# Kernel optimization log

Measured on AMD Instinct MI355X. Metric: run time of the kernel, lower is better.

The kernel has to match this reference:

```python
import jax, jax.numpy as jnp
import numpy as np

EPS = 1e-5

def _ln(x, g, b):
    m = jnp.mean(x, axis=-1, keepdims=True)
    v = jnp.var(x, axis=-1, keepdims=True)
    return (x - m) * jax.lax.rsqrt(v + EPS) * g + b

def _gelu(x):
    return jax.nn.gelu(x, approximate=False)  # torch nn.GELU default is exact erf

def setup_inputs() -> dict:
    key = jax.random.key(0)
    B, N, D, H = 4, 1024, 128, 12
    HID = H * D
    ks = jax.random.split(key, 16)
    s = lambda k, sh, fan: jax.random.normal(k, sh, jnp.float32) * (fan ** -0.5)
    return {
        "x": jax.random.normal(ks[0], (B, N, D), jnp.float32),
        # project: LN(D) -> Linear(D,HID) -> GELU -> Linear(HID,HID)
        "ln1_g": jnp.ones((D,), jnp.float32), "ln1_b": jnp.zeros((D,), jnp.float32),
        "W1": s(ks[1], (D, HID), D), "b1": jnp.zeros((HID,), jnp.float32),
        "W2": s(ks[2], (HID, HID), HID), "b2": jnp.zeros((HID,), jnp.float32),
        # shared Attention(inc=D, outc=D)
        "aln_g": jnp.ones((D,), jnp.float32), "aln_b": jnp.zeros((D,), jnp.float32),
        "Wqkv": s(ks[3], (D, 3 * D), D), "bqkv": jnp.zeros((3 * D,), jnp.float32),
        "Wl": s(ks[4], (D, D), D), "bl": jnp.zeros((D,), jnp.float32),
        # out_proj: LN(HID) -> Linear(HID, D) -> GELU
        "lno_g": jnp.ones((HID,), jnp.float32), "lno_b": jnp.zeros((HID,), jnp.float32),
        "Wo": s(ks[5], (HID, D), HID), "bo": jnp.zeros((D,), jnp.float32),
    }

def reference(x, ln1_g, ln1_b, W1, b1, W2, b2,
              aln_g, aln_b, Wqkv, bqkv, Wl, bl,
              lno_g, lno_b, Wo, bo):
    B, N, D = x.shape
    # project (dropout is identity in eval mode)
    h = _ln(x, ln1_g, ln1_b)
    h = _gelu(h @ W1 + b1)
    h = h @ W2 + b2                      # [B, N, H*D]
    H = h.shape[-1] // D
    # chunk along last dim into H features of width D; fold heads into batch
    f = h.reshape(B, N, H, D).transpose(0, 2, 1, 3).reshape(B * H, N, D)
    # shared Attention applied to each head-chunk
    a = _ln(f, aln_g, aln_b)
    qkv = a @ Wqkv + bqkv
    q, k, v = jnp.split(qkv, 3, axis=-1)
    scores = jax.nn.softmax(jnp.einsum('bnd,bmd->bnm', q, k) * (D ** -0.5), axis=-1)
    o = jnp.einsum('bnm,bmd->bnd', scores, v)
    o = o @ Wl + bl
    o = _gelu(o + f)                     # [B*H, N, D]
    # concat heads back along last dim
    feats = o.reshape(B, H, N, D).transpose(0, 2, 1, 3).reshape(B, N, H * D)
    out = _gelu(_ln(feats, lno_g, lno_b) @ Wo + bo)
    return out
```

## Files before the change

### kernel.cpp

```cpp
#include <hip/hip_runtime.h>
#include <stdint.h>

typedef unsigned short u16;
typedef __attribute__((ext_vector_type(8))) short short8;
typedef __attribute__((ext_vector_type(4))) float floatx4;

__device__ inline float b2f(u16 u) {
  union { uint32_t i; float f; } x; x.i = ((uint32_t)u) << 16; return x.f;
}
__device__ inline u16 f2b(float f) {
  union { float f; uint32_t i; } x; x.f = f;
  uint32_t r = (x.i + 0x7FFFu + ((x.i >> 16) & 1u)) >> 16;
  return (u16)r;
}
__device__ inline float gelu_f(float v) {
  return 0.5f * v * (1.0f + erff(v * 0.70710678118654752440f));
}

#define MFMA16(a, b, c) __builtin_amdgcn_mfma_f32_16x16x32_bf16((a), (b), (c), 0, 0, 0)

__device__ __forceinline__ void gl2lds16(const u16* g, u16* l) {
  __builtin_amdgcn_global_load_lds(
      (const __attribute__((address_space(1))) uint32_t*)(uintptr_t)g,
      (__attribute__((address_space(3))) uint32_t*)(uint32_t)(uintptr_t)l,
      16, 0, 0);
}

__global__ __launch_bounds__(256)
void tpose_all_kernel(const float* __restrict__ W1, const float* __restrict__ W2,
                      const float* __restrict__ Wqkv, const float* __restrict__ Wl,
                      const float* __restrict__ Wo,
                      u16* __restrict__ w1t, u16* __restrict__ w2t,
                      u16* __restrict__ wqkvt, u16* __restrict__ wlt,
                      u16* __restrict__ wot) {
  int id = blockIdx.x;
  const float* src; u16* dst; int R, C, bx, by;
  if (id < 2304)      { src = W2;   dst = w2t;   R = 1536; C = 1536; bx = (id % 48) * 32; by = (id / 48) * 32; }
  else if (id < 2496) { id -= 2304; src = W1;   dst = w1t;   R = 128;  C = 1536; bx = (id % 48) * 32; by = (id / 48) * 32; }
  else if (id < 2688) { id -= 2496; src = Wo;   dst = wot;   R = 1536; C = 128;  bx = (id % 4) * 32;  by = (id / 4) * 32; }
  else if (id < 2736) { id -= 2688; src = Wqkv; dst = wqkvt; R = 128;  C = 384;  bx = (id % 12) * 32; by = (id / 12) * 32; }
  else                { id -= 2736; src = Wl;   dst = wlt;   R = 128;  C = 128;  bx = (id % 4) * 32;  by = (id / 4) * 32; }
  __shared__ u16 t[32][33];
  int tx = threadIdx.x & 31, ty = threadIdx.x >> 5;
  for (int i = 0; i < 32; i += 8)
    t[ty + i][tx] = f2b(src[(size_t)(by + ty + i) * C + bx + tx]);
  __syncthreads();
  for (int i = 0; i < 32; i += 8)
    dst[(size_t)(bx + ty + i) * R + by + tx] = t[tx][ty + i];
}

__global__ __launch_bounds__(256)
void ln128_f32_kernel(const float* __restrict__ X, const float* __restrict__ g,
                      const float* __restrict__ bb, u16* __restrict__ Y) {
  int tid = threadIdx.x, w = tid >> 6, lane = tid & 63;
  int row = blockIdx.x * 4 + w;
  const float* xr = X + (size_t)row * 128;
  float2 xv = *(const float2*)(xr + lane * 2);
  float x0 = xv.x, x1 = xv.y;
  float s = x0 + x1, s2 = x0 * x0 + x1 * x1;
  for (int m = 1; m < 64; m <<= 1) { s += __shfl_xor(s, m, 64); s2 += __shfl_xor(s2, m, 64); }
  float mean = s * (1.0f / 128.0f);
  float var = s2 * (1.0f / 128.0f) - mean * mean;
  float rstd = 1.0f / sqrtf(var + 1e-5f);
  float2 gv = *(const float2*)(g + lane * 2);
  float2 bv = *(const float2*)(bb + lane * 2);
  float y0 = (x0 - mean) * rstd * gv.x + bv.x;
  float y1 = (x1 - mean) * rstd * gv.y + bv.y;
  *(uint32_t*)(Y + (size_t)row * 128 + lane * 2) =
      (uint32_t)f2b(y0) | ((uint32_t)f2b(y1) << 16);
}

__global__ __launch_bounds__(256)
void ln128_perm_kernel(const u16* __restrict__ X, const float* __restrict__ g,
                       const float* __restrict__ bb, u16* __restrict__ Y) {
  int tid = threadIdx.x, w = tid >> 6, lane = tid & 63;
  int rid = blockIdx.x * 4 + w;
  int bh = rid >> 10, n = rid & 1023;
  int b = bh / 12, h = bh % 12;
  const u16* xr = X + ((size_t)(b * 1024 + n)) * 1536 + h * 128;
  uint32_t u = *(const uint32_t*)(xr + lane * 2);
  float x0 = b2f(u & 0xffff), x1 = b2f(u >> 16);
  float s = x0 + x1, s2 = x0 * x0 + x1 * x1;
  for (int m = 1; m < 64; m <<= 1) { s += __shfl_xor(s, m, 64); s2 += __shfl_xor(s2, m, 64); }
  float mean = s * (1.0f / 128.0f);
  float var = s2 * (1.0f / 128.0f) - mean * mean;
  float rstd = 1.0f / sqrtf(var + 1e-5f);
  float2 gv = *(const float2*)(g + lane * 2);
  float2 bv = *(const float2*)(bb + lane * 2);
  float y0 = (x0 - mean) * rstd * gv.x + bv.x;
  float y1 = (x1 - mean) * rstd * gv.y + bv.y;
  *(uint32_t*)(Y + (size_t)rid * 128 + lane * 2) =
      (uint32_t)f2b(y0) | ((uint32_t)f2b(y1) << 16);
}

__global__ __launch_bounds__(256)
void ln1536_kernel(const u16* __restrict__ X, const float* __restrict__ g,
                   const float* __restrict__ bb, u16* __restrict__ Y) {
  int row = blockIdx.x, tid = threadIdx.x;
  const u16* xr = X + (size_t)row * 1536;
  uint32_t u0 = *(const uint32_t*)(xr + tid * 6);
  uint32_t u1 = *(const uint32_t*)(xr + tid * 6 + 2);
  uint32_t u2 = *(const uint32_t*)(xr + tid * 6 + 4);
  float v[6] = { b2f(u0 & 0xffff), b2f(u0 >> 16), b2f(u1 & 0xffff),
                 b2f(u1 >> 16),    b2f(u2 & 0xffff), b2f(u2 >> 16) };
  float s = 0.f, s2 = 0.f;
  for (int j = 0; j < 6; j++) { s += v[j]; s2 += v[j] * v[j]; }
  for (int m = 1; m < 64; m <<= 1) { s += __shfl_xor(s, m, 64); s2 += __shfl_xor(s2, m, 64); }
  __shared__ float red[8];
  int w = tid >> 6, lane = tid & 63;
  if (lane == 0) { red[w] = s; red[4 + w] = s2; }
  __syncthreads();
  s = red[0] + red[1] + red[2] + red[3];
  s2 = red[4] + red[5] + red[6] + red[7];
  float mean = s * (1.0f / 1536.0f);
  float var = s2 * (1.0f / 1536.0f) - mean * mean;
  float rstd = 1.0f / sqrtf(var + 1e-5f);
  uint32_t o[3];
  for (int p = 0; p < 3; p++) {
    int c = tid * 6 + p * 2;
    float y0 = (v[p * 2] - mean) * rstd * g[c] + bb[c];
    float y1 = (v[p * 2 + 1] - mean) * rstd * g[c + 1] + bb[c + 1];
    o[p] = (uint32_t)f2b(y0) | ((uint32_t)f2b(y1) << 16);
  }
  u16* yr = Y + (size_t)row * 1536 + tid * 6;
  *(uint32_t*)(yr) = o[0];
  *(uint32_t*)(yr + 2) = o[1];
  *(uint32_t*)(yr + 4) = o[2];
}

__global__ __launch_bounds__(256)
void qkv_kernel(const u16* __restrict__ A, const u16* __restrict__ BT,
                const float* __restrict__ bias, u16* __restrict__ qkv,
                u16* __restrict__ vT) {
  const int K = 128;
  __shared__ __align__(16) u16 abuf[128 * 32];
  __shared__ __align__(16) u16 bbuf[128 * 32];
  int tid = threadIdx.x;
  int w = tid >> 6, lane = tid & 63, ln = lane & 15, quad = lane >> 4;
  int bm = blockIdx.x * 128, bn = blockIdx.y * 128;
  int wr = w >> 1, wc = w & 1;
  floatx4 acc[4][4] = {};
  for (int k0 = 0; k0 < K; k0 += 32) {
    __syncthreads();
    for (int rd = 0; rd < 2; rd++) {
      int c = tid + rd * 256;
      int row = c >> 2, col = (c & 3) * 8;
      gl2lds16(A + (size_t)(bm + row) * K + k0 + col, abuf + c * 8);
      gl2lds16(BT + (size_t)(bn + row) * K + k0 + col, bbuf + c * 8);
    }
    __syncthreads();
    short8 af[4], bf[4];
    for (int i = 0; i < 4; i++)
      af[i] = *(const short8*)(abuf + (wr * 64 + i * 16 + ln) * 32 + quad * 8);
    for (int j = 0; j < 4; j++)
      bf[j] = *(const short8*)(bbuf + (wc * 64 + j * 16 + ln) * 32 + quad * 8);
    for (int i = 0; i < 4; i++)
      for (int j = 0; j < 4; j++)
        acc[i][j] = MFMA16(af[i], bf[j], acc[i][j]);
  }
  if (blockIdx.y < 2) {
    for (int i = 0; i < 4; i++) {
      int row0 = bm + wr * 64 + i * 16 + quad * 4;
      for (int j = 0; j < 4; j++) {
        int col = bn + wc * 64 + j * 16 + ln;
        float bv = bias[col];
        for (int r = 0; r < 4; r++)
          qkv[(size_t)(row0 + r) * 256 + col] = f2b(acc[i][j][r] + bv);
      }
    }
  } else {
    int bh = bm >> 10;
    int nb = bm & 1023;
    u16* vp = vT + (size_t)bh * 128 * 1024;
    for (int i = 0; i < 4; i++) {
      int n0 = nb + wr * 64 + i * 16 + quad * 4;
      for (int j = 0; j < 4; j++) {
        int d = wc * 64 + j * 16 + ln;
        float bv = bias[256 + d];
        u16 tmp[4];
        for (int r = 0; r < 4; r++) tmp[r] = f2b(acc[i][j][r] + bv);
        *(uint2*)(vp + (size_t)d * 1024 + n0) = *(const uint2*)tmp;
      }
    }
  }
}

template <int GELU, int RES, typename OUTT>
__global__ __launch_bounds__(256)
void gemm64_kernel(const u16* __restrict__ A, const u16* __restrict__ BT,
                   const float* __restrict__ bias, const u16* __restrict__ res,
                   OUTT* __restrict__ C, int M, int N, int K) {
  __shared__ __align__(16) u16 abuf[64 * 32];
  __shared__ __align__(16) u16 bbuf[128 * 32];
  int tid = threadIdx.x;
  int w = tid >> 6, lane = tid & 63, ln = lane & 15, quad = lane >> 4;
  int bm = blockIdx.x * 64, bn = blockIdx.y * 128;
  floatx4 acc[4][2] = {};
  for (int k0 = 0; k0 < K; k0 += 32) {
    __syncthreads();
    for (int rd = 0; rd < 2; rd++) {
      int c = tid + rd * 256;
      int row = c >> 2, col = (c & 3) * 8;
      gl2lds16(BT + (size_t)(bn + row) * K + k0 + col, bbuf + c * 8);
    }
    {
      int c = tid;
      int row = c >> 2, col = (c & 3) * 8;
      gl2lds16(A + (size_t)(bm + row) * K + k0 + col, abuf + c * 8);
    }
    __syncthreads();
    short8 af[4], bf[2];
    for (int i = 0; i < 4; i++)
      af[i] = *(const short8*)(abuf + (i * 16 + ln) * 32 + quad * 8);
    for (int j = 0; j < 2; j++)
      bf[j] = *(const short8*)(bbuf + (w * 32 + j * 16 + ln) * 32 + quad * 8);
    for (int i = 0; i < 4; i++)
      for (int j = 0; j < 2; j++)
        acc[i][j] = MFMA16(af[i], bf[j], acc[i][j]);
  }
  for (int i = 0; i < 4; i++) {
    int row0 = bm + i * 16 + quad * 4;
    for (int j = 0; j < 2; j++) {
      int col = bn + w * 32 + j * 16 + ln;
      float bv = bias[col];
      for (int r = 0; r < 4; r++) {
        float v = acc[i][j][r] + bv;
        if (RES) v += b2f(res[(size_t)(row0 + r) * N + col]);
        if (GELU) v = gelu_f(v);
        if constexpr (sizeof(OUTT) == 2)
          C[(size_t)(row0 + r) * N + col] = f2b(v);
        else
          C[(size_t)(row0 + r) * N + col] = v;
      }
    }
  }
}

template <int GELU, int RES, typename OUTT>
__global__ __launch_bounds__(256)
void gemm64b_kernel(const u16* __restrict__ A, const u16* __restrict__ BT,
                    const float* __restrict__ bias, const u16* __restrict__ res,
                    OUTT* __restrict__ C, int M, int N, int K) {
  __shared__ __align__(16) u16 abuf[2 * 64 * 32];
  __shared__ __align__(16) u16 bbuf[2 * 128 * 32];
  int tid = threadIdx.x;
  int w = tid >> 6, lane = tid & 63, ln = lane & 15, quad = lane >> 4;
  int bm = blockIdx.x * 64, bn = blockIdx.y * 128;
  floatx4 acc[4][2] = {};
  for (int k0 = 0; k0 < K; k0 += 64) {
    __syncthreads();
    for (int ks = 0; ks < 2; ks++) {
      {
        int c = tid;
        int row = c >> 2, cc = c & 3;
        gl2lds16(A + (size_t)(bm + row) * K + k0 + ks * 32 + cc * 8,
                 abuf + ks * 2048 + c * 8);
      }
      for (int rd = 0; rd < 2; rd++) {
        int c = tid + rd * 256;
        int row = c >> 2, cc = c & 3;
        gl2lds16(BT + (size_t)(bn + row) * K + k0 + ks * 32 + cc * 8,
                 bbuf + ks * 4096 + c * 8);
      }
    }
    __syncthreads();
    short8 af[2][4], bf[2][2];
    for (int ks = 0; ks < 2; ks++) {
      for (int i = 0; i < 4; i++)
        af[ks][i] = *(const short8*)(abuf + ks * 2048 + (i * 16 + ln) * 32 + quad * 8);
      for (int j = 0; j < 2; j++)
        bf[ks][j] = *(const short8*)(bbuf + ks * 4096 + (w * 32 + j * 16 + ln) * 32 + quad * 8);
    }
    for (int i = 0; i < 4; i++)
      for (int j = 0; j < 2; j++) {
        acc[i][j] = MFMA16(af[0][i], bf[0][j], acc[i][j]);
        acc[i][j] = MFMA16(af[1][i], bf[1][j], acc[i][j]);
      }
  }
  for (int i = 0; i < 4; i++) {
    int row0 = bm + i * 16 + quad * 4;
    for (int j = 0; j < 2; j++) {
      int col = bn + w * 32 + j * 16 + ln;
      float bv = bias[col];
      for (int r = 0; r < 4; r++) {
        float v = acc[i][j][r] + bv;
        if (RES) v += b2f(res[(size_t)(row0 + r) * N + col]);
        if (GELU) v = gelu_f(v);
        if constexpr (sizeof(OUTT) == 2)
          C[(size_t)(row0 + r) * N + col] = f2b(v);
        else
          C[(size_t)(row0 + r) * N + col] = v;
      }
    }
  }
}

__global__ __launch_bounds__(256)
void gemmwl_kernel(const u16* __restrict__ A, const u16* __restrict__ BT,
                   const float* __restrict__ bias, const u16* __restrict__ res,
                   u16* __restrict__ feats) {
  const int K = 128;
  __shared__ __align__(16) u16 abuf[64 * 32];
  __shared__ __align__(16) u16 bbuf[128 * 32];
  int tid = threadIdx.x;
  int w = tid >> 6, lane = tid & 63, ln = lane & 15, quad = lane >> 4;
  int bm = blockIdx.x * 64;
  floatx4 acc[4][2] = {};
  for (int k0 = 0; k0 < K; k0 += 32) {
    __syncthreads();
    for (int rd = 0; rd < 2; rd++) {
      int c = tid + rd * 256;
      int row = c >> 2, col = (c & 3) * 8;
      gl2lds16(BT + (size_t)row * K + k0 + col, bbuf + c * 8);
    }
    {
      int c = tid;
      int row = c >> 2, col = (c & 3) * 8;
      gl2lds16(A + (size_t)(bm + row) * K + k0 + col, abuf + c * 8);
    }
    __syncthreads();
    short8 af[4], bf[2];
    for (int i = 0; i < 4; i++)
      af[i] = *(const short8*)(abuf + (i * 16 + ln) * 32 + quad * 8);
    for (int j = 0; j < 2; j++)
      bf[j] = *(const short8*)(bbuf + (w * 32 + j * 16 + ln) * 32 + quad * 8);
    for (int i = 0; i < 4; i++)
      for (int j = 0; j < 2; j++)
        acc[i][j] = MFMA16(af[i], bf[j], acc[i][j]);
  }
  int bh = bm >> 10, nb = bm & 1023;
  int b = bh / 12, hh = bh % 12;
  size_t obase = ((size_t)b * 1024) * 1536 + hh * 128;
  for (int i = 0; i < 4; i++) {
    int n0 = nb + i * 16 + quad * 4;
    for (int j = 0; j < 2; j++) {
      int col = w * 32 + j * 16 + ln;
      float bv = bias[col];
      for (int r = 0; r < 4; r++) {
        size_t idx = obase + (size_t)(n0 + r) * 1536 + col;
        float v = acc[i][j][r] + bv + b2f(res[idx]);
        feats[idx] = f2b(gelu_f(v));
      }
    }
  }
}

__global__ __launch_bounds__(256)
void gemm64_part_kernel(const u16* __restrict__ A, const u16* __restrict__ BT,
                        float* __restrict__ pws, int Kfull, int kspan) {
  __shared__ __align__(16) u16 abuf[64 * 32];
  __shared__ __align__(16) u16 bbuf[128 * 32];
  int tid = threadIdx.x;
  int w = tid >> 6, lane = tid & 63, ln = lane & 15, quad = lane >> 4;
  int bm = blockIdx.x * 64;
  int kbeg = blockIdx.y * kspan, kend = kbeg + kspan;
  float* Cp = pws + (size_t)blockIdx.y * 4096 * 128;
  floatx4 acc[4][2] = {};
  for (int k0 = kbeg; k0 < kend; k0 += 32) {
    __syncthreads();
    for (int rd = 0; rd < 2; rd++) {
      int c = tid + rd * 256;
      int row = c >> 2, col = (c & 3) * 8;
      gl2lds16(BT + (size_t)row * Kfull + k0 + col, bbuf + c * 8);
    }
    {
      int c = tid;
      int row = c >> 2, col = (c & 3) * 8;
      gl2lds16(A + (size_t)(bm + row) * Kfull + k0 + col, abuf + c * 8);
    }
    __syncthreads();
    short8 af[4], bf[2];
    for (int i = 0; i < 4; i++)
      af[i] = *(const short8*)(abuf + (i * 16 + ln) * 32 + quad * 8);
    for (int j = 0; j < 2; j++)
      bf[j] = *(const short8*)(bbuf + (w * 32 + j * 16 + ln) * 32 + quad * 8);
    for (int i = 0; i < 4; i++)
      for (int j = 0; j < 2; j++)
        acc[i][j] = MFMA16(af[i], bf[j], acc[i][j]);
  }
  for (int i = 0; i < 4; i++) {
    int row0 = bm + i * 16 + quad * 4;
    for (int j = 0; j < 2; j++) {
      int col = w * 32 + j * 16 + ln;
      for (int r = 0; r < 4; r++)
        Cp[(size_t)(row0 + r) * 128 + col] = acc[i][j][r];
    }
  }
}

__global__ __launch_bounds__(256)
void combine_wo_kernel(const float* __restrict__ p, const float* __restrict__ bias,
                       float* __restrict__ out) {
  int i = blockIdx.x * 256 + threadIdx.x;
  const int SZ = 4096 * 128;
  float v = p[i] + p[i + SZ] + p[i + 2 * SZ] + p[i + 3 * SZ] + bias[i & 127];
  out[i] = gelu_f(v);
}

__global__ __launch_bounds__(256, 3)
void attn_kernel(const u16* __restrict__ qkv, const u16* __restrict__ vT,
                 u16* __restrict__ obuf) {
  int blk = blockIdx.x;
  int xcd = blk & 7, slot = blk >> 3;
  int bh = xcd * 6 + (slot >> 4);
  int qt = slot & 15;
  int tid = threadIdx.x, w = tid >> 6, lane = tid & 63, ln = lane & 15, quad = lane >> 4;
  int pair = w & 1, half = w >> 1;
  __shared__ __align__(16) u16 smem[16384 + 128];
  u16* kbuf = smem;
  u16* vbuf = smem + 8192;
  const int rs = 256;
  size_t base = (size_t)bh * 1024 * 256;
  const u16* qp = qkv + base;
  const u16* kp = qkv + base + 128;
  const u16* vp = vT + (size_t)bh * 128 * 1024;

  short8 qf[2][4];
  for (int g = 0; g < 2; g++) {
    int qrow = qt * 64 + pair * 32 + g * 16 + ln;
    for (int st = 0; st < 4; st++)
      qf[g][st] = *(const short8*)(qp + (size_t)qrow * rs + st * 32 + quad * 8);
  }

  floatx4 o[2][8] = {};
  float lsum[2] = {0.f, 0.f};
  const float K2 = 0.08838834764831845f * 1.4426950408889634f;

  int dl = ln & 3;
  int voff0 = (((quad >> 1) ^ dl) * 8) + (quad & 1) * 4;
  int voff1 = (((2 + (quad >> 1)) ^ dl) * 8) + (quad & 1) * 4;

  for (int kt = 0; kt < 16; kt++) {
    __syncthreads();
    for (int it = 0; it < 4; it++) {
      int c = it * 256 + tid;
      int st = c >> 8, key = (c >> 2) & 63, cc = c & 3;
      gl2lds16(kp + (size_t)(kt * 64 + key) * rs + st * 32 + cc * 8, kbuf + c * 8);
      int kf = c >> 9, d = (c >> 2) & 127, ccd = (c & 3) ^ (d & 3);
      gl2lds16(vp + (size_t)d * 1024 + kt * 64 + kf * 32 + ccd * 8, vbuf + c * 8);
    }
    __syncthreads();

    floatx4 s[2][2] = {};
    for (int tt = 0; tt < 2; tt++)
      for (int st = 0; st < 4; st++) {
        short8 kv = *(const short8*)(kbuf + st * 2048 +
                                     ((half * 2 + tt) * 16 + ln) * 32 + quad * 8);
        s[0][tt] = MFMA16(kv, qf[0][st], s[0][tt]);
        s[1][tt] = MFMA16(kv, qf[1][st], s[1][tt]);
      }

    short8 pfrag[2];
    for (int g = 0; g < 2; g++) {
      float p0[4], p1[4];
      for (int r = 0; r < 4; r++) {
        p0[r] = exp2f(s[g][0][r] * K2);
        p1[r] = exp2f(s[g][1][r] * K2);
        lsum[g] += p0[r] + p1[r];
      }
      uint32_t a0, a1, b0, b1;
      asm("v_cvt_pk_bf16_f32 %0, %1, %2" : "=v"(a0) : "v"(p0[0]), "v"(p0[1]));
      asm("v_cvt_pk_bf16_f32 %0, %1, %2" : "=v"(a1) : "v"(p0[2]), "v"(p0[3]));
      asm("v_cvt_pk_bf16_f32 %0, %1, %2" : "=v"(b0) : "v"(p1[0]), "v"(p1[1]));
      asm("v_cvt_pk_bf16_f32 %0, %1, %2" : "=v"(b1) : "v"(p1[2]), "v"(p1[3]));
      union { uint32_t u[4]; short8 v; } pu;
      pu.u[0] = a0; pu.u[1] = a1; pu.u[2] = b0; pu.u[3] = b1;
      pfrag[g] = pu.v;
    }

    for (int dt = 0; dt < 8; dt++) {
      const u16* vrow = vbuf + half * 4096 + (dt * 16 + ln) * 32;
      union { uint2 d2[2]; short8 v; } av;
      av.d2[0] = *(const uint2*)(vrow + voff0);
      av.d2[1] = *(const uint2*)(vrow + voff1);
      o[0][dt] = MFMA16(av.v, pfrag[0], o[0][dt]);
      o[1][dt] = MFMA16(av.v, pfrag[1], o[1][dt]);
    }
  }

  for (int g = 0; g < 2; g++) {
    lsum[g] += __shfl_xor(lsum[g], 16, 64);
    lsum[g] += __shfl_xor(lsum[g], 32, 64);
  }

  __syncthreads();
  float* mbuf = (float*)smem;
  float* lbuf = (float*)(smem + 16384);
  if (half == 1) {
    float* mp = mbuf + pair * 4096;
    for (int g = 0; g < 2; g++)
      for (int dt = 0; dt < 8; dt++)
        for (int r = 0; r < 4; r++)
          mp[(dt * 16 + quad * 4 + r) * 32 + ((g * 16 + ln + quad * 8) & 31)] = o[g][dt][r];
    if (quad == 0) {
      lbuf[pair * 32 + ln] = lsum[0];
      lbuf[pair * 32 + 16 + ln] = lsum[1];
    }
  }
  __syncthreads();
  if (half == 0) {
    float* mp = mbuf + pair * 4096;
    for (int g = 0; g < 2; g++) {
      float lt = lsum[g] + lbuf[pair * 32 + g * 16 + ln];
      float inv = 1.0f / lt;
      int n = qt * 64 + pair * 32 + g * 16 + ln;
      size_t ob = ((size_t)bh * 1024 + n) * 128;
      for (int dt = 0; dt < 8; dt++) {
        u16 tmp[4];
        for (int r = 0; r < 4; r++)
          tmp[r] = f2b((o[g][dt][r] +
                        mp[(dt * 16 + quad * 4 + r) * 32 + ((g * 16 + ln + quad * 8) & 31)]) * inv);
        *(uint2*)(obuf + ob + dt * 16 + quad * 4) = *(const uint2*)tmp;
      }
    }
  }
}

extern "C" void kernel_launch(void* const* d_in, const int* in_sizes, int n_in,
                              void* d_out, int out_size, void* d_ws, size_t ws_size,
                              hipStream_t stream) {
  (void)in_sizes; (void)n_in; (void)out_size; (void)ws_size;
  const float* x    = (const float*)d_in[0];
  const float* ln1g = (const float*)d_in[1];
  const float* ln1b = (const float*)d_in[2];
  const float* W1   = (const float*)d_in[3];
  const float* b1   = (const float*)d_in[4];
  const float* W2   = (const float*)d_in[5];
  const float* b2   = (const float*)d_in[6];
  const float* alng = (const float*)d_in[7];
  const float* alnb = (const float*)d_in[8];
  const float* Wqkv = (const float*)d_in[9];
  const float* bqkv = (const float*)d_in[10];
  const float* Wl   = (const float*)d_in[11];
  const float* bl   = (const float*)d_in[12];
  const float* lnog = (const float*)d_in[13];
  const float* lnob = (const float*)d_in[14];
  const float* Wo   = (const float*)d_in[15];
  const float* bo   = (const float*)d_in[16];
  float* out = (float*)d_out;

  char* ws = (char*)d_ws;
  size_t off = 0;
  auto alloc = [&](size_t elems) { u16* p = (u16*)(ws + off); off += elems * sizeof(u16); return p; };
  u16* w1t   = alloc((size_t)1536 * 128);
  u16* w2t   = alloc((size_t)1536 * 1536);
  u16* wqkvt = alloc((size_t)384 * 128);
  u16* wlt   = alloc((size_t)128 * 128);
  u16* wot   = alloc((size_t)128 * 1536);
  u16* lnx   = alloc((size_t)4096 * 128);
  u16* h1    = alloc((size_t)4096 * 1536);
  u16* h2    = alloc((size_t)4096 * 1536);
  u16* aln   = alloc((size_t)49152 * 128);
  u16* qkv   = alloc((size_t)49152 * 256);
  u16* obuf  = alloc((size_t)49152 * 128);
  u16* vT = h1;
  u16* feats = aln;
  u16* lnf = qkv;
  float* pws = (float*)h1;

  dim3 T(256);
  tpose_all_kernel<<<dim3(2752), T, 0, stream>>>(W1, W2, Wqkv, Wl, Wo,
                                                 w1t, w2t, wqkvt, wlt, wot);
  ln128_f32_kernel<<<dim3(4096 / 4), T, 0, stream>>>(x, ln1g, ln1b, lnx);
  gemm64_kernel<1, 0, u16><<<dim3(4096 / 64, 1536 / 128), T, 0, stream>>>(
      lnx, w1t, b1, nullptr, h1, 4096, 1536, 128);
  gemm64b_kernel<0, 0, u16><<<dim3(4096 / 64, 1536 / 128), T, 0, stream>>>(
      h1, w2t, b2, nullptr, h2, 4096, 1536, 1536);
  ln128_perm_kernel<<<dim3(49152 / 4), T, 0, stream>>>(h2, alng, alnb, aln);
  qkv_kernel<<<dim3(49152 / 128, 3), T, 0, stream>>>(aln, wqkvt, bqkv, qkv, vT);
  attn_kernel<<<dim3(768), T, 0, stream>>>(qkv, vT, obuf);
  gemmwl_kernel<<<dim3(49152 / 64), T, 0, stream>>>(obuf, wlt, bl, h2, feats);
  ln1536_kernel<<<dim3(4096), T, 0, stream>>>(feats, lnog, lnob, lnf);
  gemm64_part_kernel<<<dim3(4096 / 64, 4), T, 0, stream>>>(lnf, wot, pws, 1536, 384);
  combine_wo_kernel<<<dim3(4096 * 128 / 256), T, 0, stream>>>(pws, bo, out);
}
```

Measured before the change: 251.6 us.

## Prefetch next K/V tiles into LDS with double-buffered V in attention

The attention loop now issues the global-to-LDS loads for the next key tile while the current tile is being computed. K fragments are read into registers right after the barrier, so the single K buffer can be refilled early, and V gets two LDS buffers used in alternation. The aim is to hide global load latency behind the MFMA and exp work instead of stalling on a load-then-sync at the top of every iteration. LDS use per block grows by 16 KB, which could limit occupancy at three blocks per CU, and holding the K fragments raises register pressure.

```diff
diff --git a/kernel.cpp b/kernel.cpp
--- a/kernel.cpp
+++ b/kernel.cpp
@@ -406,9 +406,9 @@
   int qt = slot & 15;
   int tid = threadIdx.x, w = tid >> 6, lane = tid & 63, ln = lane & 15, quad = lane >> 4;
   int pair = w & 1, half = w >> 1;
-  __shared__ __align__(16) u16 smem[16384 + 128];
+  __shared__ __align__(16) u16 smem[24576 + 128];
   u16* kbuf = smem;
-  u16* vbuf = smem + 8192;
+  u16* vbufs = smem + 8192;
   const int rs = 256;
   size_t base = (size_t)bh * 1024 * 256;
   const u16* qp = qkv + base;
@@ -430,24 +430,45 @@
   int voff0 = (((quad >> 1) ^ dl) * 8) + (quad & 1) * 4;
   int voff1 = (((2 + (quad >> 1)) ^ dl) * 8) + (quad & 1) * 4;
 
-  for (int kt = 0; kt < 16; kt++) {
-    __syncthreads();
+  auto STAGE_K = [&](int kt) {
     for (int it = 0; it < 4; it++) {
       int c = it * 256 + tid;
       int st = c >> 8, key = (c >> 2) & 63, cc = c & 3;
       gl2lds16(kp + (size_t)(kt * 64 + key) * rs + st * 32 + cc * 8, kbuf + c * 8);
+    }
+  };
+  auto STAGE_V = [&](int kt, int buf) {
+    u16* vb = vbufs + buf * 8192;
+    for (int it = 0; it < 4; it++) {
+      int c = it * 256 + tid;
       int kf = c >> 9, d = (c >> 2) & 127, ccd = (c & 3) ^ (d & 3);
-      gl2lds16(vp + (size_t)d * 1024 + kt * 64 + kf * 32 + ccd * 8, vbuf + c * 8);
-    }
-    __syncthreads();
+      gl2lds16(vp + (size_t)d * 1024 + kt * 64 + kf * 32 + ccd * 8, vb + c * 8);
+    }
+  };
+
+  STAGE_K(0);
+  STAGE_V(0, 0);
+
+  for (int kt = 0; kt < 16; kt++) {
+    __syncthreads();
+
+    short8 kfr[2][4];
+    for (int tt = 0; tt < 2; tt++)
+      for (int st = 0; st < 4; st++)
+        kfr[tt][st] = *(const short8*)(kbuf + st * 2048 +
+                                       ((half * 2 + tt) * 16 + ln) * 32 + quad * 8);
+    __syncthreads();
+
+    if (kt < 15) {
+      STAGE_K(kt + 1);
+      STAGE_V(kt + 1, (kt + 1) & 1);
+    }
 
     floatx4 s[2][2] = {};
     for (int tt = 0; tt < 2; tt++)
       for (int st = 0; st < 4; st++) {
-        short8 kv = *(const short8*)(kbuf + st * 2048 +
-                                     ((half * 2 + tt) * 16 + ln) * 32 + quad * 8);
-        s[0][tt] = MFMA16(kv, qf[0][st], s[0][tt]);
-        s[1][tt] = MFMA16(kv, qf[1][st], s[1][tt]);
+        s[0][tt] = MFMA16(kfr[tt][st], qf[0][st], s[0][tt]);
+        s[1][tt] = MFMA16(kfr[tt][st], qf[1][st], s[1][tt]);
       }
 
     short8 pfrag[2];
@@ -468,8 +489,9 @@
       pfrag[g] = pu.v;
     }
 
+    const u16* vb = vbufs + (kt & 1) * 8192;
     for (int dt = 0; dt < 8; dt++) {
-      const u16* vrow = vbuf + half * 4096 + (dt * 16 + ln) * 32;
+      const u16* vrow = vb + half * 4096 + (dt * 16 + ln) * 32;
       union { uint2 d2[2]; short8 v; } av;
       av.d2[0] = *(const uint2*)(vrow + voff0);
       av.d2[1] = *(const uint2*)(vrow + voff1);
```

Measured after the change: 249.6 us. About the same (-0.8%).
